# Performance work log

Hardware: AMD Instinct MI355X
Metric: run time of the kernel (lower is better)

Reference implementation:

```python
import jax, jax.numpy as jnp
import numpy as np

DECAY = 0.9
THRESH = 1.0
ALPHA = 4.0  # surrogate-gradient sharpness for the LIF heaviside
NUM_HEADS = 8


def lif(x):
    """LIF neuron over leading time axis: mem = decay*mem + x; spike = H(mem - thresh); soft reset.
    Forward emits the hard spike; a sigmoid surrogate carries the gradient (straight-through).
    x: (T, M, D) -> spikes (T, M, D)."""
    def step(mem, xt):
        mem = DECAY * mem + xt
        sg = jax.nn.sigmoid(ALPHA * (mem - THRESH))
        hard = (mem >= THRESH).astype(xt.dtype)
        spike = sg + jax.lax.stop_gradient(hard - sg)
        mem = mem - spike * THRESH
        return mem, spike
    _, spikes = jax.lax.scan(step, jnp.zeros_like(x[0]), x)
    return spikes


def setup_inputs() -> dict:
    key = jax.random.key(0)
    ks = jax.random.split(key, 6)
    T, B, N, D = 4, 16, 1024, 512
    s = 1.0 / np.sqrt(D)
    return {
        "x_seq": jax.random.normal(ks[0], (T, B, N, D), jnp.float32),
        "Wq": (jax.random.normal(ks[1], (D, D), jnp.float32) * s),
        "Wk": (jax.random.normal(ks[2], (D, D), jnp.float32) * s),
        "Wv": (jax.random.normal(ks[3], (D, D), jnp.float32) * s),
        "Wp": (jax.random.normal(ks[4], (D, D), jnp.float32) * s),
        "bp": jnp.zeros((D,), jnp.float32),
    }


def reference(x_seq, Wq, Wk, Wv, Wp, bp):
    T, B, N, D = x_seq.shape
    hd = D // NUM_HEADS
    xf = x_seq.reshape(T, B * N, D)
    # projections (no bias) + LIF spiking, then the module's view into (T,B,H,N,hd)
    q = lif(xf @ Wq.T).reshape(T, B, NUM_HEADS, N, hd)
    k = lif(xf @ Wk.T).reshape(T, B, NUM_HEADS, N, hd)
    v = lif(xf @ Wv.T).reshape(T, B, NUM_HEADS, N, hd)
    # causal linear attention: elementwise kv, cumulative sum over time (kv_state is None on fresh module)
    context = jnp.cumsum(k * v, axis=0)
    out = (q * context).reshape(T, B * N, D)
    return (out @ Wp.T + bp).reshape(T, B, N, D)
```

## Files before the change

### kernel.cpp

```cpp
#include <hip/hip_runtime.h>
#include <hip/hip_bf16.h>
#include <stdint.h>

#define T_ 4
#define M_ 16384
#define D_ 512
#define R_ (T_ * M_)
#define EPS_TRIG 1e-4f

typedef short bf16x8 __attribute__((ext_vector_type(8)));
typedef float f32x4  __attribute__((ext_vector_type(4)));
typedef unsigned short us8 __attribute__((ext_vector_type(8)));

static __device__ __forceinline__ void split2bf16(float x, unsigned short& h, unsigned short& l) {
    unsigned int u = __float_as_uint(x);
    h = (unsigned short)(u >> 16);
    float r = x - __uint_as_float(u & 0xFFFF0000u);
    unsigned int v = __float_as_uint(r);
    l = (unsigned short)((v + 0x7FFFu + ((v >> 16) & 1u)) >> 16);
}

static __device__ __forceinline__ void gload_lds16(const void* g, void* l) {
    __builtin_amdgcn_global_load_lds(
        (const __attribute__((address_space(1))) unsigned int*)g,
        (__attribute__((address_space(3))) unsigned int*)l,
        16, 0, 0);
}

__global__ __launch_bounds__(256) void split_w_tiled(
    const float* __restrict__ Wq, const float* __restrict__ Wk, const float* __restrict__ Wv,
    unsigned short* __restrict__ Wt)
{
    const int flat = blockIdx.x * 256 + threadIdx.x;
    const int dd   = flat & 63;
    const int rest = flat >> 6;
    const int wj   = rest % 24;
    const int bk   = rest / 24;
    const int kbi  = bk & 15;
    const int bd   = bk >> 4;
    const int z    = wj % 3;
    const int hg   = wj / 3;
    const int hl   = hg >> 2;
    const int g    = hg & 3;

    const float* src = ((z == 0) ? Wq : (z == 1) ? Wk : Wv)
                       + (size_t)(bd * 64 + dd) * D_ + kbi * 32 + g * 8;
    float4 a = *reinterpret_cast<const float4*>(src);
    float4 b = *reinterpret_cast<const float4*>(src + 4);

    us8 hv, lv;
    unsigned short hh, ll;
    split2bf16(a.x, hh, ll); hv[0] = hh; lv[0] = ll;
    split2bf16(a.y, hh, ll); hv[1] = hh; lv[1] = ll;
    split2bf16(a.z, hh, ll); hv[2] = hh; lv[2] = ll;
    split2bf16(a.w, hh, ll); hv[3] = hh; lv[3] = ll;
    split2bf16(b.x, hh, ll); hv[4] = hh; lv[4] = ll;
    split2bf16(b.y, hh, ll); hv[5] = hh; lv[5] = ll;
    split2bf16(b.z, hh, ll); hv[6] = hh; lv[6] = ll;
    split2bf16(b.w, hh, ll); hv[7] = hh; lv[7] = ll;

    *reinterpret_cast<us8*>((char*)Wt + (size_t)flat * 16) = hl ? lv : hv;
}

__global__ __launch_bounds__(256) void split_wp_tiled(
    const float* __restrict__ Wp, unsigned short* __restrict__ WpT)
{
    const int flat = blockIdx.x * 256 + threadIdx.x;
    const int dd   = flat & 63;
    const int g    = (flat >> 6) & 3;
    const int kbi  = (flat >> 8) & 15;
    const int bd   = flat >> 12;

    const float* src = Wp + (size_t)(bd * 64 + dd) * D_ + kbi * 32 + g * 8;
    float4 a = *reinterpret_cast<const float4*>(src);
    float4 b = *reinterpret_cast<const float4*>(src + 4);

    us8 hv, lv;
    unsigned short hh, ll;
    split2bf16(a.x, hh, ll); hv[0] = hh; lv[0] = ll;
    split2bf16(a.y, hh, ll); hv[1] = hh; lv[1] = ll;
    split2bf16(a.z, hh, ll); hv[2] = hh; lv[2] = ll;
    split2bf16(a.w, hh, ll); hv[3] = hh; lv[3] = ll;
    split2bf16(b.x, hh, ll); hv[4] = hh; lv[4] = ll;
    split2bf16(b.y, hh, ll); hv[5] = hh; lv[5] = ll;
    split2bf16(b.z, hh, ll); hv[6] = hh; lv[6] = ll;
    split2bf16(b.w, hh, ll); hv[7] = hh; lv[7] = ll;

    char* chunk = (char*)WpT + (size_t)(bd * 16 + kbi) * 8192;
    *reinterpret_cast<us8*>(chunk + g * 1024 + dd * 16)        = hv;
    *reinterpret_cast<us8*>(chunk + 4096 + g * 1024 + dd * 16) = lv;
}

__global__ __launch_bounds__(256) void split_x_tiled3(
    const float* __restrict__ X, unsigned short* __restrict__ Xt)
{
    const int bmp  = blockIdx.x;
    const int tid  = threadIdx.x;
    const int rowp = tid >> 2;
    const int g    = tid & 3;
    const int t    = rowp >> 4;
    const int mm   = rowp & 15;

    const float* srow = X + (size_t)(t * M_ + bmp * 16 + mm) * D_;

    for (int kb = 0; kb < 16; kb++) {
        const float* src = srow + kb * 32 + g * 8;
        float4 a = *reinterpret_cast<const float4*>(src);
        float4 b = *reinterpret_cast<const float4*>(src + 4);

        us8 hv, lv;
        unsigned short hh, ll;
        split2bf16(a.x, hh, ll); hv[0] = hh; lv[0] = ll;
        split2bf16(a.y, hh, ll); hv[1] = hh; lv[1] = ll;
        split2bf16(a.z, hh, ll); hv[2] = hh; lv[2] = ll;
        split2bf16(a.w, hh, ll); hv[3] = hh; lv[3] = ll;
        split2bf16(b.x, hh, ll); hv[4] = hh; lv[4] = ll;
        split2bf16(b.y, hh, ll); hv[5] = hh; lv[5] = ll;
        split2bf16(b.z, hh, ll); hv[6] = hh; lv[6] = ll;
        split2bf16(b.w, hh, ll); hv[7] = hh; lv[7] = ll;

        char* chunk = (char*)Xt + (size_t)(bmp * 16 + kb) * 8192;
        *reinterpret_cast<us8*>(chunk + g * 1024 + rowp * 16)        = hv;
        *reinterpret_cast<us8*>(chunk + 4096 + g * 1024 + rowp * 16) = lv;
    }
}

__global__ __launch_bounds__(256, 4) void proj_lif_attn_v4(
    const float* __restrict__ X,
    const float* __restrict__ Wq, const float* __restrict__ Wk, const float* __restrict__ Wv,
    const unsigned short* __restrict__ XtS, const unsigned short* __restrict__ WtS,
    unsigned char* __restrict__ attn)
{
    __shared__ unsigned short Xs[2][4096];

    const int tid  = threadIdx.x;
    const int lane = tid & 63;
    const int wsub = tid >> 6;
    const int la   = lane & 15;
    const int lq   = lane >> 4;

    const int n   = blockIdx.y * 8 + blockIdx.x;
    const int bd  = (n >> 3) & 7;
    const int bmp = (n & 7) * 128 + (n >> 6);

    f32x4 acc[3][T_];
    #pragma unroll
    for (int z = 0; z < 3; z++)
        #pragma unroll
        for (int t = 0; t < T_; t++)
            acc[z][t] = (f32x4){0.f, 0.f, 0.f, 0.f};

    const char* xsrc0 = (const char*)XtS + (size_t)(bmp * 16) * 8192 + wsub * 2048 + lane * 16;
    const char* wb    = (const char*)WtS + (size_t)(bd * 16) * 24576 + lq * 3072 + wsub * 256 + la * 16;
    char* xd0 = (char*)&Xs[0][0] + wsub * 2048;
    char* xd1 = (char*)&Xs[1][0] + wsub * 2048;

    gload_lds16(xsrc0,        xd0);
    gload_lds16(xsrc0 + 1024, xd0 + 1024);
    __syncthreads();

    for (int kbi = 0; kbi < 16; kbi++) {
        const int cur = kbi & 1;

        bf16x8 bh[3], bl[3];
        #pragma unroll
        for (int z = 0; z < 3; z++) {
            const char* p = wb + (size_t)kbi * 24576 + z * 1024;
            bh[z] = *reinterpret_cast<const bf16x8*>(p);
            bl[z] = *reinterpret_cast<const bf16x8*>(p + 12288);
        }

        if (kbi < 15) {
            const char* xs = xsrc0 + (size_t)(kbi + 1) * 8192;
            char* xd = cur ? xd0 : xd1;
            gload_lds16(xs,        xd);
            gload_lds16(xs + 1024, xd + 1024);
        }

        const char* Xc = (const char*)&Xs[cur][0];
        #pragma unroll
        for (int t = 0; t < T_; t++) {
            const int ab = lq * 1024 + (t * 16 + la) * 16;
            bf16x8 ah = *reinterpret_cast<const bf16x8*>(Xc + ab);
            bf16x8 al = *reinterpret_cast<const bf16x8*>(Xc + 4096 + ab);
            #pragma unroll
            for (int z = 0; z < 3; z++) {
                acc[z][t] = __builtin_amdgcn_mfma_f32_16x16x32_bf16(ah, bh[z], acc[z][t], 0, 0, 0);
                acc[z][t] = __builtin_amdgcn_mfma_f32_16x16x32_bf16(ah, bl[z], acc[z][t], 0, 0, 0);
                acc[z][t] = __builtin_amdgcn_mfma_f32_16x16x32_bf16(al, bh[z], acc[z][t], 0, 0, 0);
            }
        }
        __syncthreads();
    }

    const int d = bd * 64 + wsub * 16 + la;
    #pragma unroll
    for (int i = 0; i < 4; i++) {
        const int m = bmp * 16 + lq * 4 + i;
        int sp[3][T_];
        int zrisky = 0;
        #pragma unroll
        for (int z = 0; z < 3; z++) {
            float mem = 0.f;
            #pragma unroll
            for (int t = 0; t < T_; t++) {
                mem = 0.9f * mem + acc[z][t][i];
                if (fabsf(mem - 1.0f) < EPS_TRIG) zrisky |= (1 << z);
                const int sb = (mem >= 1.0f) ? 1 : 0;
                sp[z][t] = sb;
                mem -= (float)sb;
            }
        }
        unsigned long long ball = __ballot(zrisky != 0);
        while (ball) {
            const int src = (int)__builtin_ctzll(ball);
            ball &= ball - 1;
            const int bits = __shfl(zrisky, src);
            const int m_s  = bmp * 16 + (src >> 4) * 4 + i;
            const int d_s  = bd * 64 + wsub * 16 + (src & 15);
            #pragma unroll
            for (int z = 0; z < 3; z++) {
                if (!(bits & (1 << z))) continue;
                const float* Wrow = ((z == 0) ? Wq : (z == 1) ? Wk : Wv) + (size_t)d_s * D_;
                float4 w0 = *reinterpret_cast<const float4*>(Wrow + lane * 8);
                float4 w1 = *reinterpret_cast<const float4*>(Wrow + lane * 8 + 4);
                double pre[T_];
                #pragma unroll
                for (int t = 0; t < T_; t++) {
                    const float* xrow = X + (size_t)(t * M_ + m_s) * D_ + lane * 8;
                    float4 x0 = *reinterpret_cast<const float4*>(xrow);
                    float4 x1 = *reinterpret_cast<const float4*>(xrow + 4);
                    double p = (double)x0.x * (double)w0.x + (double)x0.y * (double)w0.y
                             + (double)x0.z * (double)w0.z + (double)x0.w * (double)w0.w
                             + (double)x1.x * (double)w1.x + (double)x1.y * (double)w1.y
                             + (double)x1.z * (double)w1.z + (double)x1.w * (double)w1.w;
                    #pragma unroll
                    for (int off = 32; off > 0; off >>= 1)
                        p += __shfl_xor(p, off, 64);
                    pre[t] = p;
                }
                double dm = 0.0;
                int spz[T_];
                #pragma unroll
                for (int t = 0; t < T_; t++) {
                    dm = 0.9 * dm + pre[t];
                    const int sb = (dm >= 1.0) ? 1 : 0;
                    spz[t] = sb;
                    dm -= (double)sb;
                }
                if (lane == src) {
                    #pragma unroll
                    for (int t = 0; t < T_; t++) sp[z][t] = spz[t];
                }
            }
        }
        int ctx = 0;
        #pragma unroll
        for (int t = 0; t < T_; t++) {
            ctx += sp[1][t] & sp[2][t];
            attn[(size_t)(t * M_ + m) * D_ + d] = (unsigned char)(sp[0][t] ? ctx : 0);
        }
    }
}

__global__ __launch_bounds__(256, 4) void attn_out_gemm_v2(
    const unsigned char* __restrict__ A,
    const unsigned short* __restrict__ WpT,
    const float*         __restrict__ bp,
    float* __restrict__ out)
{
    __shared__ unsigned short As[128 * 40];

    const int tid  = threadIdx.x;
    const int lane = tid & 63;
    const int wsub = tid >> 6;
    const int la   = lane & 15;
    const int lq   = lane >> 4;

    const int n  = blockIdx.y * 8 + blockIdx.x;
    const int bd = (n >> 3) & 7;
    const int bm = (n & 7) * 64 + (n >> 6);

    f32x4 acc[8];
    #pragma unroll
    for (int s = 0; s < 8; s++) acc[s] = (f32x4){0.f, 0.f, 0.f, 0.f};

    int arow[4], akq[4];
    #pragma unroll
    for (int i = 0; i < 4; i++) {
        const int j = tid + i * 256;
        arow[i] = j >> 3;
        akq[i]  = (j & 7) * 4;
    }

    uchar4 rA[4];
    #pragma unroll
    for (int i = 0; i < 4; i++)
        rA[i] = *reinterpret_cast<const uchar4*>(
            A + (size_t)(bm * 128 + arow[i]) * D_ + akq[i]);

    for (int kb = 0; kb < 16; kb++) {
        #pragma unroll
        for (int i = 0; i < 4; i++) {
            ushort4 h;
            h.x = (unsigned short)(__float_as_uint((float)rA[i].x) >> 16);
            h.y = (unsigned short)(__float_as_uint((float)rA[i].y) >> 16);
            h.z = (unsigned short)(__float_as_uint((float)rA[i].z) >> 16);
            h.w = (unsigned short)(__float_as_uint((float)rA[i].w) >> 16);
            *reinterpret_cast<ushort4*>(&As[arow[i] * 40 + akq[i]]) = h;
        }
        uchar4 rN[4];
        if (kb < 15) {
            #pragma unroll
            for (int i = 0; i < 4; i++)
                rN[i] = *reinterpret_cast<const uchar4*>(
                    A + (size_t)(bm * 128 + arow[i]) * D_ + (kb + 1) * 32 + akq[i]);
        }
        __syncthreads();

        const char* wp = (const char*)WpT + (size_t)(bd * 16 + kb) * 8192
                         + lq * 1024 + (wsub * 16 + la) * 16;
        bf16x8 bh = *reinterpret_cast<const bf16x8*>(wp);
        bf16x8 bl = *reinterpret_cast<const bf16x8*>(wp + 4096);

        #pragma unroll
        for (int s = 0; s < 8; s++) {
            bf16x8 a = *reinterpret_cast<const bf16x8*>(&As[(s * 16 + la) * 40 + lq * 8]);
            acc[s] = __builtin_amdgcn_mfma_f32_16x16x32_bf16(a, bh, acc[s], 0, 0, 0);
            acc[s] = __builtin_amdgcn_mfma_f32_16x16x32_bf16(a, bl, acc[s], 0, 0, 0);
        }
        __syncthreads();

        #pragma unroll
        for (int i = 0; i < 4; i++) rA[i] = rN[i];
    }

    const int d = bd * 64 + wsub * 16 + la;
    const float bias = bp[d];
    #pragma unroll
    for (int s = 0; s < 8; s++)
        #pragma unroll
        for (int i = 0; i < 4; i++) {
            const int m = bm * 128 + s * 16 + lq * 4 + i;
            out[(size_t)m * D_ + d] = acc[s][i] + bias;
        }
}

extern "C" void kernel_launch(void* const* d_in, const int* in_sizes, int n_in,
                              void* d_out, int out_size, void* d_ws, size_t ws_size,
                              hipStream_t stream) {
    const float* x  = (const float*)d_in[0];
    const float* wq = (const float*)d_in[1];
    const float* wk = (const float*)d_in[2];
    const float* wv = (const float*)d_in[3];
    const float* wp = (const float*)d_in[4];
    const float* bp = (const float*)d_in[5];

    unsigned char*  attn = (unsigned char*)d_ws;
    unsigned short* Wt   = (unsigned short*)((char*)d_ws + 33554432);
    unsigned short* WpT  = (unsigned short*)((char*)d_ws + 36700160);
    unsigned short* Xt   = (unsigned short*)((char*)d_ws + 37748736);

    dim3 blk(256);
    split_w_tiled <<<dim3(768),  blk, 0, stream>>>(wq, wk, wv, Wt);
    split_wp_tiled<<<dim3(128),  blk, 0, stream>>>(wp, WpT);
    split_x_tiled3<<<dim3(1024), blk, 0, stream>>>(x, Xt);

    dim3 g1(8, 1024);
    proj_lif_attn_v4<<<g1, blk, 0, stream>>>(x, wq, wk, wv, Xt, Wt, attn);

    dim3 g2(8, 512);
    attn_out_gemm_v2<<<g2, blk, 0, stream>>>(attn, WpT, bp, (float*)d_out);
}
```

Before: 559.8 us.

## Software-pipeline weight and activation loads in both GEMM kernels with ping-pong buffers

The projection kernel's K loop is unrolled by two. Each step now holds two register sets of weight fragments, so the weight global loads for the next K block are issued before the MFMAs of the current block. The output GEMM gains a second LDS buffer for A and double-buffered weight registers, which lets the store and load of the next tile overlap the current MFMA phase. The goal is to hide global-load latency behind compute. The cost is higher register and LDS use, which may reduce occupancy at the launch bound of 4.

```diff
diff --git a/kernel.cpp b/kernel.cpp
--- a/kernel.cpp
+++ b/kernel.cpp
@@ -125,7 +125,7 @@
     }
 }
 
-__global__ __launch_bounds__(256, 4) void proj_lif_attn_v4(
+__global__ __launch_bounds__(256, 4) void proj_lif_attn_v5(
     const float* __restrict__ X,
     const float* __restrict__ Wq, const float* __restrict__ Wk, const float* __restrict__ Wv,
     const unsigned short* __restrict__ XtS, const unsigned short* __restrict__ WtS,
@@ -155,41 +155,50 @@
     char* xd0 = (char*)&Xs[0][0] + wsub * 2048;
     char* xd1 = (char*)&Xs[1][0] + wsub * 2048;
 
-    gload_lds16(xsrc0,        xd0);
-    gload_lds16(xsrc0 + 1024, xd0 + 1024);
-    __syncthreads();
-
-    for (int kbi = 0; kbi < 16; kbi++) {
-        const int cur = kbi & 1;
-
-        bf16x8 bh[3], bl[3];
+    bf16x8 whA[3], wlA[3], whB[3], wlB[3];
+
+    auto loadW = [&](bf16x8 (&wh)[3], bf16x8 (&wl)[3], int kbi) {
+        const char* p = wb + (size_t)kbi * 24576;
         #pragma unroll
         for (int z = 0; z < 3; z++) {
-            const char* p = wb + (size_t)kbi * 24576 + z * 1024;
-            bh[z] = *reinterpret_cast<const bf16x8*>(p);
-            bl[z] = *reinterpret_cast<const bf16x8*>(p + 12288);
-        }
-
-        if (kbi < 15) {
-            const char* xs = xsrc0 + (size_t)(kbi + 1) * 8192;
-            char* xd = cur ? xd0 : xd1;
-            gload_lds16(xs,        xd);
-            gload_lds16(xs + 1024, xd + 1024);
-        }
-
-        const char* Xc = (const char*)&Xs[cur][0];
+            wh[z] = *reinterpret_cast<const bf16x8*>(p + z * 1024);
+            wl[z] = *reinterpret_cast<const bf16x8*>(p + z * 1024 + 12288);
+        }
+    };
+    auto stageX = [&](int kbi, char* xd) {
+        const char* xs = xsrc0 + (size_t)kbi * 8192;
+        gload_lds16(xs,        xd);
+        gload_lds16(xs + 1024, xd + 1024);
+    };
+    auto mfmaPhase = [&](const unsigned short* Xc, const bf16x8 (&wh)[3], const bf16x8 (&wl)[3]) {
         #pragma unroll
         for (int t = 0; t < T_; t++) {
             const int ab = lq * 1024 + (t * 16 + la) * 16;
-            bf16x8 ah = *reinterpret_cast<const bf16x8*>(Xc + ab);
-            bf16x8 al = *reinterpret_cast<const bf16x8*>(Xc + 4096 + ab);
+            bf16x8 ah = *reinterpret_cast<const bf16x8*>((const char*)Xc + ab);
+            bf16x8 al = *reinterpret_cast<const bf16x8*>((const char*)Xc + 4096 + ab);
             #pragma unroll
             for (int z = 0; z < 3; z++) {
-                acc[z][t] = __builtin_amdgcn_mfma_f32_16x16x32_bf16(ah, bh[z], acc[z][t], 0, 0, 0);
-                acc[z][t] = __builtin_amdgcn_mfma_f32_16x16x32_bf16(ah, bl[z], acc[z][t], 0, 0, 0);
-                acc[z][t] = __builtin_amdgcn_mfma_f32_16x16x32_bf16(al, bh[z], acc[z][t], 0, 0, 0);
+                acc[z][t] = __builtin_amdgcn_mfma_f32_16x16x32_bf16(ah, wh[z], acc[z][t], 0, 0, 0);
+                acc[z][t] = __builtin_amdgcn_mfma_f32_16x16x32_bf16(ah, wl[z], acc[z][t], 0, 0, 0);
+                acc[z][t] = __builtin_amdgcn_mfma_f32_16x16x32_bf16(al, wh[z], acc[z][t], 0, 0, 0);
             }
         }
+    };
+
+    stageX(0, xd0);
+    loadW(whA, wlA, 0);
+    __syncthreads();
+
+    for (int kp = 0; kp < 8; kp++) {
+        stageX(2 * kp + 1, xd1);
+        loadW(whB, wlB, 2 * kp + 1);
+        mfmaPhase(&Xs[0][0], whA, wlA);
+        __syncthreads();
+        if (kp < 7) {
+            stageX(2 * kp + 2, xd0);
+            loadW(whA, wlA, 2 * kp + 2);
+        }
+        mfmaPhase(&Xs[1][0], whB, wlB);
         __syncthreads();
     }
 
@@ -263,13 +272,13 @@
     }
 }
 
-__global__ __launch_bounds__(256, 4) void attn_out_gemm_v2(
+__global__ __launch_bounds__(256, 4) void attn_out_gemm_v3(
     const unsigned char* __restrict__ A,
     const unsigned short* __restrict__ WpT,
     const float*         __restrict__ bp,
     float* __restrict__ out)
 {
-    __shared__ unsigned short As[128 * 40];
+    __shared__ unsigned short As[2][128 * 40];
 
     const int tid  = threadIdx.x;
     const int lane = tid & 63;
@@ -292,47 +301,62 @@
         arow[i] = j >> 3;
         akq[i]  = (j & 7) * 4;
     }
-
-    uchar4 rA[4];
-    #pragma unroll
-    for (int i = 0; i < 4; i++)
-        rA[i] = *reinterpret_cast<const uchar4*>(
-            A + (size_t)(bm * 128 + arow[i]) * D_ + akq[i]);
-
-    for (int kb = 0; kb < 16; kb++) {
+    const unsigned char* Ab = A + (size_t)(bm * 128) * D_;
+
+    uchar4 S[4], P[4];
+    bf16x8 whA, wlA, whB, wlB;
+
+    auto loadA = [&](uchar4 (&r)[4], int kb) {
+        #pragma unroll
+        for (int i = 0; i < 4; i++)
+            r[i] = *reinterpret_cast<const uchar4*>(
+                Ab + (size_t)arow[i] * D_ + kb * 32 + akq[i]);
+    };
+    auto storeA = [&](int buf, const uchar4 (&r)[4]) {
         #pragma unroll
         for (int i = 0; i < 4; i++) {
             ushort4 h;
-            h.x = (unsigned short)(__float_as_uint((float)rA[i].x) >> 16);
-            h.y = (unsigned short)(__float_as_uint((float)rA[i].y) >> 16);
-            h.z = (unsigned short)(__float_as_uint((float)rA[i].z) >> 16);
-            h.w = (unsigned short)(__float_as_uint((float)rA[i].w) >> 16);
-            *reinterpret_cast<ushort4*>(&As[arow[i] * 40 + akq[i]]) = h;
-        }
-        uchar4 rN[4];
-        if (kb < 15) {
-            #pragma unroll
-            for (int i = 0; i < 4; i++)
-                rN[i] = *reinterpret_cast<const uchar4*>(
-                    A + (size_t)(bm * 128 + arow[i]) * D_ + (kb + 1) * 32 + akq[i]);
-        }
+            h.x = (unsigned short)(__float_as_uint((float)r[i].x) >> 16);
+            h.y = (unsigned short)(__float_as_uint((float)r[i].y) >> 16);
+            h.z = (unsigned short)(__float_as_uint((float)r[i].z) >> 16);
+            h.w = (unsigned short)(__float_as_uint((float)r[i].w) >> 16);
+            *reinterpret_cast<ushort4*>(&As[buf][arow[i] * 40 + akq[i]]) = h;
+        }
+    };
+    auto loadW = [&](bf16x8& wh, bf16x8& wl, int kb) {
+        const char* p = (const char*)WpT + (size_t)(bd * 16 + kb) * 8192
+                        + lq * 1024 + (wsub * 16 + la) * 16;
+        wh = *reinterpret_cast<const bf16x8*>(p);
+        wl = *reinterpret_cast<const bf16x8*>(p + 4096);
+    };
+    auto mfmaPhase = [&](int buf, const bf16x8& wh, const bf16x8& wl) {
+        #pragma unroll
+        for (int s = 0; s < 8; s++) {
+            bf16x8 a = *reinterpret_cast<const bf16x8*>(&As[buf][(s * 16 + la) * 40 + lq * 8]);
+            acc[s] = __builtin_amdgcn_mfma_f32_16x16x32_bf16(a, wh, acc[s], 0, 0, 0);
+            acc[s] = __builtin_amdgcn_mfma_f32_16x16x32_bf16(a, wl, acc[s], 0, 0, 0);
+        }
+    };
+
+    loadA(S, 0);
+    storeA(0, S);
+    loadW(whA, wlA, 0);
+    loadA(S, 1);
+    __syncthreads();
+
+    for (int kp = 0; kp < 8; kp++) {
+        storeA(1, S);
+        loadW(whB, wlB, 2 * kp + 1);
+        if (kp < 7) loadA(P, 2 * kp + 2);
+        mfmaPhase(0, whA, wlA);
         __syncthreads();
-
-        const char* wp = (const char*)WpT + (size_t)(bd * 16 + kb) * 8192
-                         + lq * 1024 + (wsub * 16 + la) * 16;
-        bf16x8 bh = *reinterpret_cast<const bf16x8*>(wp);
-        bf16x8 bl = *reinterpret_cast<const bf16x8*>(wp + 4096);
-
-        #pragma unroll
-        for (int s = 0; s < 8; s++) {
-            bf16x8 a = *reinterpret_cast<const bf16x8*>(&As[(s * 16 + la) * 40 + lq * 8]);
-            acc[s] = __builtin_amdgcn_mfma_f32_16x16x32_bf16(a, bh, acc[s], 0, 0, 0);
-            acc[s] = __builtin_amdgcn_mfma_f32_16x16x32_bf16(a, bl, acc[s], 0, 0, 0);
-        }
+        if (kp < 7) {
+            storeA(0, P);
+            loadW(whA, wlA, 2 * kp + 2);
+            loadA(S, 2 * kp + 3);
+        }
+        mfmaPhase(1, whB, wlB);
         __syncthreads();
-
-        #pragma unroll
-        for (int i = 0; i < 4; i++) rA[i] = rN[i];
     }
 
     const int d = bd * 64 + wsub * 16 + la;
@@ -367,8 +391,8 @@
     split_x_tiled3<<<dim3(1024), blk, 0, stream>>>(x, Xt);
 
     dim3 g1(8, 1024);
-    proj_lif_attn_v4<<<g1, blk, 0, stream>>>(x, wq, wk, wv, Xt, Wt, attn);
+    proj_lif_attn_v5<<<g1, blk, 0, stream>>>(x, wq, wk, wv, Xt, Wt, attn);
 
     dim3 g2(8, 512);
-    attn_out_gemm_v2<<<g2, blk, 0, stream>>>(attn, WpT, bp, (float*)d_out);
-}
+    attn_out_gemm_v3<<<g2, blk, 0, stream>>>(attn, WpT, bp, (float*)d_out);
+}
```

Result: no change. 549.3 us (-1.9%).
